# Kernel optimization log

Measured on AMD Instinct MI355X. Metric: run time of the kernel, lower is better.

The kernel has to match this reference:

```python
import jax, jax.numpy as jnp
import numpy as np
from jax import lax

DILATIONS = (1, 3, 9, 9, 3, 1)  # six mid blocks after the 1x1 input conv


def bilinear_sample(fm, verts):
    # fm: [B,H,W,C]; verts: [B,N,2] in [-1,1]; axis 0 of verts maps to H, axis 1 to W.
    # Matches jax.scipy.ndimage.map_coordinates(order=1, mode='constant'):
    # each out-of-bounds corner contributes 0.
    B, H, W, C = fm.shape
    scale = jnp.array([H - 1, W - 1], fm.dtype) / 2.0
    coords = (verts + 1.0) * scale  # [B,N,2]
    vy, vx = coords[..., 0], coords[..., 1]
    y0 = jnp.floor(vy)
    x0 = jnp.floor(vx)
    wy = (vy - y0)[..., None]
    wx = (vx - x0)[..., None]
    y0i = y0.astype(jnp.int32)
    x0i = x0.astype(jnp.int32)
    fm_flat = fm.reshape(B, H * W, C)

    def corner(yi, xi):
        valid = (yi >= 0) & (yi < H) & (xi >= 0) & (xi < W)
        idx = jnp.clip(yi, 0, H - 1) * W + jnp.clip(xi, 0, W - 1)  # [B,N]
        vals = jnp.take_along_axis(fm_flat, idx[..., None], axis=1)  # [B,N,C]
        return jnp.where(valid[..., None], vals, jnp.zeros((), fm.dtype))

    return ((1 - wy) * (1 - wx) * corner(y0i, x0i)
            + (1 - wy) * wx * corner(y0i, x0i + 1)
            + wy * (1 - wx) * corner(y0i + 1, x0i)
            + wy * wx * corner(y0i + 1, x0i + 1))


def conv1d(x, w, b, dil):
    # x: [B,N,Cin], w: [K,Cin,Cout]; flax nnx.Conv default: stride 1, SAME padding.
    out = lax.conv_general_dilated(x, w, (1,), 'SAME', rhs_dilation=(dil,),
                                   dimension_numbers=('NWC', 'WIO', 'NWC'))
    return out if b is None else out + b


def setup_inputs() -> dict:
    key = jax.random.key(0)
    ks = jax.random.split(key, 8)
    B, N, H, W, Cf, Ch = 16, 1024, 256, 256, 126, 512
    D = Cf + 2
    vertices = jax.random.uniform(ks[0], (B, N, 2), jnp.float32, -1.0, 1.0)
    feature_map = jax.random.normal(ks[1], (B, H, W, Cf), jnp.float32)
    w0 = jax.random.normal(ks[2], (1, D, Ch), jnp.float32) / np.float32(np.sqrt(D))
    b0 = jnp.zeros((Ch,), jnp.float32)
    ws = jax.random.normal(ks[3], (6, 3, Ch, Ch), jnp.float32) / np.float32(np.sqrt(3 * Ch))
    bs = jnp.zeros((6, Ch), jnp.float32)
    w_off = jax.random.normal(ks[4], (1, Ch, 2), jnp.float32) / np.float32(np.sqrt(Ch))
    return {"vertices": vertices, "feature_map": feature_map,
            "w0": w0, "b0": b0, "ws": ws, "bs": bs, "w_off": w_off}


def reference(vertices, feature_map, w0, b0, ws, bs, w_off):
    feat = bilinear_sample(feature_map, vertices)          # [B,N,Cf]
    x = jnp.concatenate([feat, vertices], axis=-1)         # [B,N,Cf+2]
    x = jax.nn.relu(conv1d(x, w0, b0, 1))                  # 1x1 input conv
    for i, dil in enumerate(DILATIONS):                    # fixed 6-layer stack
        x = jax.nn.relu(conv1d(x, ws[i], bs[i], dil))
    return conv1d(x, w_off, None, 1)                       # [B,N,2] offsets
```

## Files before the change

kernel.cpp:

```cpp
#include <hip/hip_runtime.h>

typedef __attribute__((ext_vector_type(4))) float f32x4;
typedef __attribute__((ext_vector_type(8))) _Float16 f16x8;

#define BM 128
#define BK 64

#define OFF_W0T 0
#define OFF_WT  131072
#define OFF_X0  (OFF_WT + 6*512*1536*2)
#define OFF_Y0  (OFF_X0 + 16384*128*2)
#define OFF_Y1  (OFF_Y0 + 16*1056*512*2)

__device__ __forceinline__ void load_lds16(const void* g, void* s) {
    __builtin_amdgcn_global_load_lds(
        (const __attribute__((address_space(1))) void*)g,
        (__attribute__((address_space(3))) void*)s, 16, 0, 0);
}

__global__ __launch_bounds__(256)
void wprep(const float* __restrict__ ws, const float* __restrict__ w0,
           _Float16* __restrict__ wt, _Float16* __restrict__ w0t)
{
    __shared__ float t[64][65];
    const int tid = threadIdx.x;
    const int tr = tid >> 6;
    const int tc = tid & 63;
    const int z = blockIdx.z;
    if (z < 18) {
        const int l = z / 3, tp = z % 3;
        const float* src = ws + (size_t)z * 512 * 512;
        const int ci0 = blockIdx.y * 64, co0 = blockIdx.x * 64;
        #pragma unroll
        for (int i = 0; i < 16; ++i) { int r = i*4 + tr; t[r][tc] = src[(ci0 + r)*512 + co0 + tc]; }
        __syncthreads();
        _Float16* dst = wt + (size_t)l * 512 * 1536;
        #pragma unroll
        for (int i = 0; i < 16; ++i) { int r = i*4 + tr; dst[(co0 + r)*1536 + tp*512 + ci0 + tc] = (_Float16)t[tc][r]; }
    } else {
        if (blockIdx.y >= 2) return;
        const int ci0 = blockIdx.y * 64, co0 = blockIdx.x * 64;
        #pragma unroll
        for (int i = 0; i < 16; ++i) { int r = i*4 + tr; t[r][tc] = w0[(ci0 + r)*512 + co0 + tc]; }
        __syncthreads();
        #pragma unroll
        for (int i = 0; i < 16; ++i) { int r = i*4 + tr; w0t[(co0 + r)*128 + ci0 + tc] = (_Float16)t[tc][r]; }
    }
}

__global__ __launch_bounds__(256)
void zeropad(_Float16* __restrict__ Y0, _Float16* __restrict__ Y1)
{
    const int i = blockIdx.x * 256 + threadIdx.x;
    const unsigned c2   = i & 255;
    const unsigned t2   = ((unsigned)i) >> 8;
    const unsigned prow = t2 & 31;
    const unsigned b    = (t2 >> 5) & 15;
    const unsigned buf  = t2 >> 9;
    const unsigned row  = prow < 16 ? prow : (1024 + prow);
    unsigned* p = (unsigned*)(buf ? Y1 : Y0);
    p[((size_t)b * 1056 + row) * 256 + c2] = 0u;
}

__global__ __launch_bounds__(256)
void sample_kernel(const float* __restrict__ verts, const float* __restrict__ fm,
                   _Float16* __restrict__ X0)
{
    const int p = blockIdx.x * 4 + (threadIdx.x >> 6);
    const int lane = threadIdx.x & 63;
    const int b = p >> 10;
    const float vy = verts[p*2], vx = verts[p*2 + 1];
    const float cy = (vy + 1.f) * 127.5f;
    const float cx = (vx + 1.f) * 127.5f;
    const float fy = floorf(cy), fx = floorf(cx);
    const int y0 = (int)fy, x0 = (int)fx;
    const float wy = cy - fy, wx = cx - fx;
    float w00 = (1.f - wy) * (1.f - wx), w01 = (1.f - wy) * wx;
    float w10 = wy * (1.f - wx),         w11 = wy * wx;
    const bool vy0 = (unsigned)y0 < 256u, vy1 = (unsigned)(y0 + 1) < 256u;
    const bool vx0 = (unsigned)x0 < 256u, vx1 = (unsigned)(x0 + 1) < 256u;
    w00 = (vy0 && vx0) ? w00 : 0.f;
    w01 = (vy0 && vx1) ? w01 : 0.f;
    w10 = (vy1 && vx0) ? w10 : 0.f;
    w11 = (vy1 && vx1) ? w11 : 0.f;
    const int yc0 = min(max(y0, 0), 255), yc1 = min(max(y0 + 1, 0), 255);
    const int xc0 = min(max(x0, 0), 255), xc1 = min(max(x0 + 1, 0), 255);
    const float* base = fm + (size_t)b * (256 * 256 * 126);
    const float* p00 = base + (yc0 * 256 + xc0) * 126;
    const float* p01 = base + (yc0 * 256 + xc1) * 126;
    const float* p10 = base + (yc1 * 256 + xc0) * 126;
    const float* p11 = base + (yc1 * 256 + xc1) * 126;
    _Float16* xr = X0 + (size_t)p * 128;
    for (int c = lane; c < 126; c += 64) {
        float a = w00 * p00[c] + w01 * p01[c] + w10 * p10[c] + w11 * p11[c];
        xr[c] = (_Float16)a;
    }
    if (lane < 2) xr[126 + lane] = (_Float16)(lane ? vx : vy);
}

template<int KTOT>
__global__ __launch_bounds__(256)
void conv_gemm(const _Float16* __restrict__ A, int a_row_stride, int a_batch_stride,
               const _Float16* __restrict__ WT, const float* __restrict__ bias,
               _Float16* __restrict__ Out, int o_row_stride, int o_batch_stride,
               int dil)
{
    __shared__ _Float16 Ald[BM * BK];
    __shared__ _Float16 Bld[BM * BK];
    const int tid  = threadIdx.x;
    const int wid  = tid >> 6;
    const int lane = tid & 63;
    const int b    = blockIdx.x >> 3;
    const int n0   = (blockIdx.x & 7) * BM;
    const int co0  = blockIdx.y * BM;
    const int wm   = wid >> 1, wn = wid & 1;

    const _Float16* Ab = A + (size_t)b * a_batch_stride + (size_t)n0 * a_row_stride;

    f32x4 acc[4][4] = {};

    const int srow = lane >> 3;
    const int scol = (lane & 7) * 8;

    for (int ks = 0; ks < KTOT / BK; ++ks) {
        int ci0, shift;
        if (KTOT == 128) { ci0 = ks * 64; shift = 0; }
        else             { int t = ks >> 3; ci0 = (ks & 7) * 64; shift = (t - 1) * dil; }
        const _Float16* Arow = Ab + (long)shift * a_row_stride + ci0 + scol;
        const _Float16* Brow = WT + (size_t)co0 * KTOT + ks * 64 + scol;
        #pragma unroll
        for (int i = 0; i < 4; ++i) {
            const int r0 = wid * 32 + i * 8;
            load_lds16(Arow + (size_t)(r0 + srow) * a_row_stride, &Ald[r0 * BK]);
            load_lds16(Brow + (size_t)(r0 + srow) * KTOT,         &Bld[r0 * BK]);
        }
        __syncthreads();
        #pragma unroll
        for (int kf = 0; kf < 2; ++kf) {
            f16x8 af[4], bfr[4];
            #pragma unroll
            for (int f = 0; f < 4; ++f) {
                af[f]  = *(const f16x8*)&Ald[(wm*64 + f*16 + (lane & 15)) * BK + kf*32 + (lane >> 4) * 8];
                bfr[f] = *(const f16x8*)&Bld[(wn*64 + f*16 + (lane & 15)) * BK + kf*32 + (lane >> 4) * 8];
            }
            #pragma unroll
            for (int m = 0; m < 4; ++m)
                #pragma unroll
                for (int n = 0; n < 4; ++n)
                    acc[m][n] = __builtin_amdgcn_mfma_f32_16x16x32_f16(af[m], bfr[n], acc[m][n], 0, 0, 0);
        }
        __syncthreads();
    }

    _Float16* Ob = Out + (size_t)b * o_batch_stride + (size_t)n0 * o_row_stride;
    #pragma unroll
    for (int n = 0; n < 4; ++n) {
        const int co = co0 + wn*64 + n*16 + (lane & 15);
        const float bv = bias[co];
        #pragma unroll
        for (int m = 0; m < 4; ++m) {
            #pragma unroll
            for (int j = 0; j < 4; ++j) {
                const int row = wm*64 + m*16 + (lane >> 4)*4 + j;
                float v = acc[m][n][j] + bv;
                v = fmaxf(v, 0.f);
                Ob[(size_t)row * o_row_stride + co] = (_Float16)v;
            }
        }
    }
}

#define NT8 24
__global__ __launch_bounds__(512, 2)
void conv_gemm8(const _Float16* __restrict__ A, const _Float16* __restrict__ WT,
                const float* __restrict__ bias, _Float16* __restrict__ Out, int dil)
{
    extern __shared__ _Float16 smem[];
    _Float16* Ald = smem;
    _Float16* Bld = smem + 3 * 256 * 64;

    const int tid  = threadIdx.x;
    const int wid  = tid >> 6;
    const int lane = tid & 63;
    const int wm   = wid >> 1;
    const int wn   = wid & 1;

    const int orig = blockIdx.x;
    const int swz  = (orig & 7) * 32 + (orig >> 3);
    const int nblk = swz & 3;
    const int mblk = swz >> 2;
    const int b     = mblk >> 2;
    const int n0row = (mblk & 3) * 256;
    const int co0   = nblk * 128;

    const _Float16* Ab = A + (size_t)b * (1056 * 512) + (size_t)n0row * 512;

    const int srow = lane >> 3;
    const int scol = (((lane & 7) ^ (lane >> 3)) << 3);

    f32x4 acc[4][4] = {};

    auto stageA = [&](int kt, int c, int ci0, int shift) {
        const int grow = 64 * c + 8 * wid + srow;
        const _Float16* src = Ab + (long)(grow + shift) * 512 + ci0 + scol;
        _Float16* dst = Ald + (kt % 3) * (256 * 64) + (64 * c + 8 * wid) * 64;
        load_lds16(src, dst);
    };
    auto stageB = [&](int kt, int c, int kk) {
        const int grow = 64 * c + 8 * wid + srow;
        const _Float16* src = WT + (size_t)(co0 + grow) * 1536 + kk + scol;
        _Float16* dst = Bld + (kt % 3) * (128 * 64) + (64 * c + 8 * wid) * 64;
        load_lds16(src, dst);
    };
    auto kinfo = [&](int ks, int& ci0, int& shift) {
        const int t = ks >> 3; ci0 = (ks & 7) * 64; shift = (t - 1) * dil;
    };

    {
        int ci0, sh;
        kinfo(0, ci0, sh);
        stageA(0, 0, ci0, sh); stageA(0, 1, ci0, sh); stageA(0, 2, ci0, sh); stageA(0, 3, ci0, sh);
        stageB(0, 0, 0); stageB(0, 1, 0);
        kinfo(1, ci0, sh);
        stageA(1, 0, ci0, sh); stageA(1, 1, ci0, sh); stageA(1, 2, ci0, sh); stageA(1, 3, ci0, sh);
        stageB(1, 0, 64); stageB(1, 1, 64);
    }

    for (int kt = 0; kt < NT8; ++kt) {
        if (kt < NT8 - 1) asm volatile("s_waitcnt vmcnt(6)" ::: "memory");
        else              asm volatile("s_waitcnt vmcnt(0)" ::: "memory");
        __builtin_amdgcn_s_barrier();

        const _Float16* Abuf = Ald + (kt % 3) * (256 * 64);
        const _Float16* Bbuf = Bld + (kt % 3) * (128 * 64);
        const bool do_stage = (kt + 2 < NT8);
        int nci0 = 0, nsh = 0;
        if (do_stage) kinfo(kt + 2, nci0, nsh);

        f16x8 bfr[4][2];
        #pragma unroll
        for (int p = 0; p < 2; ++p) {
            f16x8 af[2][2];
            #pragma unroll
            for (int mf = 0; mf < 2; ++mf) {
                const int row = wm * 64 + (p * 2 + mf) * 16 + (lane & 15);
                #pragma unroll
                for (int kf = 0; kf < 2; ++kf) {
                    const int slot = (kf * 4 + (lane >> 4)) ^ (row & 7);
                    af[mf][kf] = *(const f16x8*)&Abuf[row * 64 + slot * 8];
                }
            }
            if (p == 0) {
                #pragma unroll
                for (int nf = 0; nf < 4; ++nf) {
                    const int row = wn * 64 + nf * 16 + (lane & 15);
                    #pragma unroll
                    for (int kf = 0; kf < 2; ++kf) {
                        const int slot = (kf * 4 + (lane >> 4)) ^ (row & 7);
                        bfr[nf][kf] = *(const f16x8*)&Bbuf[row * 64 + slot * 8];
                    }
                }
            }
            if (do_stage) {
                if (p == 0) {
                    stageA(kt + 2, 0, nci0, nsh);
                    stageA(kt + 2, 1, nci0, nsh);
                    stageA(kt + 2, 2, nci0, nsh);
                } else {
                    stageA(kt + 2, 3, nci0, nsh);
                    stageB(kt + 2, 0, (kt + 2) * 64);
                    stageB(kt + 2, 1, (kt + 2) * 64);
                }
            }
            __builtin_amdgcn_s_barrier();
            __builtin_amdgcn_s_setprio(1);
            #pragma unroll
            for (int mf = 0; mf < 2; ++mf)
                #pragma unroll
                for (int nf = 0; nf < 4; ++nf)
                    #pragma unroll
                    for (int kf = 0; kf < 2; ++kf)
                        acc[p * 2 + mf][nf] = __builtin_amdgcn_mfma_f32_16x16x32_f16(
                            af[mf][kf], bfr[nf][kf], acc[p * 2 + mf][nf], 0, 0, 0);
            __builtin_amdgcn_s_setprio(0);
            __builtin_amdgcn_s_barrier();
        }
    }

    _Float16* Ob = Out + (size_t)b * (1056 * 512) + (size_t)n0row * 512;
    #pragma unroll
    for (int nf = 0; nf < 4; ++nf) {
        const int co = co0 + wn * 64 + nf * 16 + (lane & 15);
        const float bv = bias[co];
        #pragma unroll
        for (int m = 0; m < 4; ++m) {
            #pragma unroll
            for (int j = 0; j < 4; ++j) {
                const int row = wm * 64 + m * 16 + (lane >> 4) * 4 + j;
                float v = acc[m][nf][j] + bv;
                v = fmaxf(v, 0.f);
                Ob[(size_t)row * 512 + co] = (_Float16)v;
            }
        }
    }
}

__global__ __launch_bounds__(256)
void final_conv(const _Float16* __restrict__ Y, const float* __restrict__ woff,
                float* __restrict__ out)
{
    const int r = blockIdx.x * 4 + (threadIdx.x >> 6);
    const int lane = threadIdx.x & 63;
    const int b = r >> 10, n = r & 1023;
    const _Float16* yp = Y + ((size_t)b * 1056 + n) * 512 + lane * 8;
    f16x8 yv = *(const f16x8*)yp;
    const int ci0 = lane * 8;
    float s0 = 0.f, s1 = 0.f;
    #pragma unroll
    for (int e = 0; e < 8; ++e) {
        float y = (float)yv[e];
        s0 += y * woff[(ci0 + e) * 2 + 0];
        s1 += y * woff[(ci0 + e) * 2 + 1];
    }
    #pragma unroll
    for (int off = 32; off; off >>= 1) {
        s0 += __shfl_down(s0, off);
        s1 += __shfl_down(s1, off);
    }
    if (lane == 0) { out[r*2] = s0; out[r*2 + 1] = s1; }
}

extern "C" void kernel_launch(void* const* d_in, const int* in_sizes, int n_in,
                              void* d_out, int out_size, void* d_ws, size_t ws_size,
                              hipStream_t stream)
{
    const float* verts = (const float*)d_in[0];
    const float* fm    = (const float*)d_in[1];
    const float* w0    = (const float*)d_in[2];
    const float* b0    = (const float*)d_in[3];
    const float* ws    = (const float*)d_in[4];
    const float* bs    = (const float*)d_in[5];
    const float* woff  = (const float*)d_in[6];
    float* out = (float*)d_out;

    char* wsp = (char*)d_ws;
    _Float16* W0T = (_Float16*)(wsp + OFF_W0T);
    _Float16* WT  = (_Float16*)(wsp + OFF_WT);
    _Float16* X0  = (_Float16*)(wsp + OFF_X0);
    _Float16* Y0  = (_Float16*)(wsp + OFF_Y0);
    _Float16* Y1  = (_Float16*)(wsp + OFF_Y1);
    _Float16* Y0i = Y0 + 16 * 512;
    _Float16* Y1i = Y1 + 16 * 512;

    hipFuncSetAttribute(reinterpret_cast<const void*>(&conv_gemm8),
                        hipFuncAttributeMaxDynamicSharedMemorySize, 147456);

    wprep<<<dim3(8, 8, 19), 256, 0, stream>>>(ws, w0, WT, W0T);
    zeropad<<<1024, 256, 0, stream>>>(Y0, Y1);
    sample_kernel<<<4096, 256, 0, stream>>>(verts, fm, X0);

    conv_gemm<128><<<dim3(128, 4), 256, 0, stream>>>(
        X0, 128, 1024 * 128, W0T, b0, Y0i, 512, 1056 * 512, 1);

    const int DIL[6] = {1, 3, 9, 9, 3, 1};
    _Float16* bufs[2] = {Y0i, Y1i};
    for (int l = 0; l < 6; ++l) {
        conv_gemm8<<<256, 512, 147456, stream>>>(
            bufs[l & 1],
            WT + (size_t)l * 512 * 1536, bs + (size_t)l * 512,
            bufs[(l + 1) & 1], DIL[l]);
    }

    final_conv<<<4096, 256, 0, stream>>>(bufs[0], woff, out);
}
```

Before: 211.5 us.

## Use 4 waves per block with 128x64 warp tiles in dilated conv GEMM

The dilated conv GEMM now runs 256 threads (4 waves, 2x2) per 256x128 tile, so each wave computes a 128x64 sub-tile with 32 accumulator fragments instead of 16. The split ping-pong schedule with intra-iteration barriers and setprio is replaced by one barrier per k-step: the whole next-next tile is staged up front, then all fragments are loaded and all MFMAs issued. This cuts barrier and synchronisation overhead and raises MFMA work per LDS read. In exchange register pressure is much higher and there are fewer waves to hide latency, since the 144 KB of LDS still allows only one block per CU.

```diff
diff --git a/kernel.cpp b/kernel.cpp
--- a/kernel.cpp
+++ b/kernel.cpp
@@ -171,7 +171,7 @@
 }
 
 #define NT8 24
-__global__ __launch_bounds__(512, 2)
+__global__ __launch_bounds__(256, 1)
 void conv_gemm8(const _Float16* __restrict__ A, const _Float16* __restrict__ WT,
                 const float* __restrict__ bias, _Float16* __restrict__ Out, int dil)
 {
@@ -198,93 +198,71 @@
     const int srow = lane >> 3;
     const int scol = (((lane & 7) ^ (lane >> 3)) << 3);
 
-    f32x4 acc[4][4] = {};
-
-    auto stageA = [&](int kt, int c, int ci0, int shift) {
-        const int grow = 64 * c + 8 * wid + srow;
-        const _Float16* src = Ab + (long)(grow + shift) * 512 + ci0 + scol;
-        _Float16* dst = Ald + (kt % 3) * (256 * 64) + (64 * c + 8 * wid) * 64;
-        load_lds16(src, dst);
+    f32x4 acc[8][4] = {};
+
+    auto stageA = [&](int kt, int j, int ci0, int shift) {
+        const int rb = 64 * wid + 8 * j;
+        const _Float16* src = Ab + (long)(rb + srow + shift) * 512 + ci0 + scol;
+        load_lds16(src, Ald + (kt % 3) * (256 * 64) + rb * 64);
     };
-    auto stageB = [&](int kt, int c, int kk) {
-        const int grow = 64 * c + 8 * wid + srow;
-        const _Float16* src = WT + (size_t)(co0 + grow) * 1536 + kk + scol;
-        _Float16* dst = Bld + (kt % 3) * (128 * 64) + (64 * c + 8 * wid) * 64;
-        load_lds16(src, dst);
+    auto stageB = [&](int kt, int j, int kk) {
+        const int rb = 32 * wid + 8 * j;
+        const _Float16* src = WT + (size_t)(co0 + rb + srow) * 1536 + kk + scol;
+        load_lds16(src, Bld + (kt % 3) * (128 * 64) + rb * 64);
     };
     auto kinfo = [&](int ks, int& ci0, int& shift) {
         const int t = ks >> 3; ci0 = (ks & 7) * 64; shift = (t - 1) * dil;
     };
-
-    {
-        int ci0, sh;
-        kinfo(0, ci0, sh);
-        stageA(0, 0, ci0, sh); stageA(0, 1, ci0, sh); stageA(0, 2, ci0, sh); stageA(0, 3, ci0, sh);
-        stageB(0, 0, 0); stageB(0, 1, 0);
-        kinfo(1, ci0, sh);
-        stageA(1, 0, ci0, sh); stageA(1, 1, ci0, sh); stageA(1, 2, ci0, sh); stageA(1, 3, ci0, sh);
-        stageB(1, 0, 64); stageB(1, 1, 64);
-    }
+    auto stage_tile = [&](int kt) {
+        int ci0, sh; kinfo(kt, ci0, sh);
+        #pragma unroll
+        for (int j = 0; j < 8; ++j) stageA(kt, j, ci0, sh);
+        #pragma unroll
+        for (int j = 0; j < 4; ++j) stageB(kt, j, kt * 64);
+    };
+
+    stage_tile(0);
+    stage_tile(1);
 
     for (int kt = 0; kt < NT8; ++kt) {
-        if (kt < NT8 - 1) asm volatile("s_waitcnt vmcnt(6)" ::: "memory");
+        if (kt < NT8 - 1) asm volatile("s_waitcnt vmcnt(12)" ::: "memory");
         else              asm volatile("s_waitcnt vmcnt(0)" ::: "memory");
         __builtin_amdgcn_s_barrier();
 
+        if (kt + 2 < NT8) stage_tile(kt + 2);
+
         const _Float16* Abuf = Ald + (kt % 3) * (256 * 64);
         const _Float16* Bbuf = Bld + (kt % 3) * (128 * 64);
-        const bool do_stage = (kt + 2 < NT8);
-        int nci0 = 0, nsh = 0;
-        if (do_stage) kinfo(kt + 2, nci0, nsh);
 
         f16x8 bfr[4][2];
         #pragma unroll
-        for (int p = 0; p < 2; ++p) {
-            f16x8 af[2][2];
-            #pragma unroll
-            for (int mf = 0; mf < 2; ++mf) {
-                const int row = wm * 64 + (p * 2 + mf) * 16 + (lane & 15);
+        for (int nf = 0; nf < 4; ++nf) {
+            const int row = wn * 64 + nf * 16 + (lane & 15);
+            #pragma unroll
+            for (int kf = 0; kf < 2; ++kf) {
+                const int slot = (kf * 4 + (lane >> 4)) ^ (row & 7);
+                bfr[nf][kf] = *(const f16x8*)&Bbuf[row * 64 + slot * 8];
+            }
+        }
+        f16x8 af[8][2];
+        #pragma unroll
+        for (int mf = 0; mf < 8; ++mf) {
+            const int row = wm * 128 + mf * 16 + (lane & 15);
+            #pragma unroll
+            for (int kf = 0; kf < 2; ++kf) {
+                const int slot = (kf * 4 + (lane >> 4)) ^ (row & 7);
+                af[mf][kf] = *(const f16x8*)&Abuf[row * 64 + slot * 8];
+            }
+        }
+
+        #pragma unroll
+        for (int mf = 0; mf < 8; ++mf)
+            #pragma unroll
+            for (int nf = 0; nf < 4; ++nf)
                 #pragma unroll
-                for (int kf = 0; kf < 2; ++kf) {
-                    const int slot = (kf * 4 + (lane >> 4)) ^ (row & 7);
-                    af[mf][kf] = *(const f16x8*)&Abuf[row * 64 + slot * 8];
-                }
-            }
-            if (p == 0) {
-                #pragma unroll
-                for (int nf = 0; nf < 4; ++nf) {
-                    const int row = wn * 64 + nf * 16 + (lane & 15);
-                    #pragma unroll
-                    for (int kf = 0; kf < 2; ++kf) {
-                        const int slot = (kf * 4 + (lane >> 4)) ^ (row & 7);
-                        bfr[nf][kf] = *(const f16x8*)&Bbuf[row * 64 + slot * 8];
-                    }
-                }
-            }
-            if (do_stage) {
-                if (p == 0) {
-                    stageA(kt + 2, 0, nci0, nsh);
-                    stageA(kt + 2, 1, nci0, nsh);
-                    stageA(kt + 2, 2, nci0, nsh);
-                } else {
-                    stageA(kt + 2, 3, nci0, nsh);
-                    stageB(kt + 2, 0, (kt + 2) * 64);
-                    stageB(kt + 2, 1, (kt + 2) * 64);
-                }
-            }
-            __builtin_amdgcn_s_barrier();
-            __builtin_amdgcn_s_setprio(1);
-            #pragma unroll
-            for (int mf = 0; mf < 2; ++mf)
-                #pragma unroll
-                for (int nf = 0; nf < 4; ++nf)
-                    #pragma unroll
-                    for (int kf = 0; kf < 2; ++kf)
-                        acc[p * 2 + mf][nf] = __builtin_amdgcn_mfma_f32_16x16x32_f16(
-                            af[mf][kf], bfr[nf][kf], acc[p * 2 + mf][nf], 0, 0, 0);
-            __builtin_amdgcn_s_setprio(0);
-            __builtin_amdgcn_s_barrier();
-        }
+                for (int kf = 0; kf < 2; ++kf)
+                    acc[mf][nf] = __builtin_amdgcn_mfma_f32_16x16x32_f16(
+                        af[mf][kf], bfr[nf][kf], acc[mf][nf], 0, 0, 0);
     }
 
     _Float16* Ob = Out + (size_t)b * (1056 * 512) + (size_t)n0row * 512;
@@ -293,11 +271,11 @@
         const int co = co0 + wn * 64 + nf * 16 + (lane & 15);
         const float bv = bias[co];
         #pragma unroll
-        for (int m = 0; m < 4; ++m) {
+        for (int mf = 0; mf < 8; ++mf) {
             #pragma unroll
             for (int j = 0; j < 4; ++j) {
-                const int row = wm * 64 + m * 16 + (lane >> 4) * 4 + j;
-                float v = acc[m][nf][j] + bv;
+                const int row = wm * 128 + mf * 16 + (lane >> 4) * 4 + j;
+                float v = acc[mf][nf][j] + bv;
                 v = fmaxf(v, 0.f);
                 Ob[(size_t)row * 512 + co] = (_Float16)v;
             }
@@ -365,7 +343,7 @@
     const int DIL[6] = {1, 3, 9, 9, 3, 1};
     _Float16* bufs[2] = {Y0i, Y1i};
     for (int l = 0; l < 6; ++l) {
-        conv_gemm8<<<256, 512, 147456, stream>>>(
+        conv_gemm8<<<256, 256, 147456, stream>>>(
             bufs[l & 1],
             WT + (size_t)l * 512 * 1536, bs + (size_t)l * 512,
             bufs[(l + 1) & 1], DIL[l]);
```

Measured after the change: 259.4 us. 1.23x slower.
